# Kernel optimization log

Hardware: AMD Instinct MI355X
Metric: run time of the kernel (lower is better)

Reference implementation:

```python
import jax, jax.numpy as jnp
import numpy as np
from jax import lax

GRID = 200      # _FIXED_GRID_LEN
SOFT_K = 50.0   # _SOFT_MASK_K
BN_EPS = 1e-5


def setup_inputs() -> dict:
    key = jax.random.key(0)
    ks = jax.random.split(key, 12)
    B, L = 8192, 2001
    f32 = jnp.float32
    inp = {
        'phase': jax.random.uniform(ks[0], (B, L), f32, -1.0, 1.0),
        'primary_flux': 0.01 * jax.random.normal(ks[1], (B, L), f32),
        'secondary_flux': 0.01 * jax.random.normal(ks[2], (B, L), f32),
        'odd_even_diff': 0.01 * jax.random.normal(ks[3], (B, L), f32),
        # TaylorGateLayerV8 params
        'A': jnp.asarray(0.01, f32),
        'Bp': jnp.asarray(1.0, f32),
        't0': jnp.asarray(0.0, f32),
        # BatchNorm1d(4), eval mode (running stats)
        'bn_gamma': jnp.ones((4,), f32),
        'bn_beta': jnp.zeros((4,), f32),
        'bn_mean': jnp.zeros((4,), f32),
        'bn_var': jnp.ones((4,), f32),
        # Conv1d(4,8,7) / Conv1d(8,16,5)
        'conv1_w': 0.1 * jax.random.normal(ks[4], (8, 4, 7), f32),
        'conv1_b': jnp.zeros((8,), f32),
        'conv2_w': 0.1 * jax.random.normal(ks[5], (16, 8, 5), f32),
        'conv2_b': jnp.zeros((16,), f32),
        # Linear(21, 1)
        'fc_w': 0.1 * jax.random.normal(ks[6], (1, 21), f32),
        'fc_b': jnp.zeros((1,), f32),
    }
    return inp


def _conv1d(x, w, b, pad):
    # x: (B, C, L), w: (O, C, K)
    y = lax.conv_general_dilated(x, w, window_strides=(1,), padding=[(pad, pad)],
                                 dimension_numbers=('NCH', 'OIH', 'NCH'))
    return y + b[None, :, None]


def _interp_linear_ac(x, out_len):
    # torch F.interpolate(mode='linear', align_corners=True) on (B, L) -> (B, out_len)
    L = x.shape[1]
    pos = jnp.linspace(0.0, L - 1.0, out_len)
    i0 = jnp.floor(pos).astype(jnp.int32)
    i1 = jnp.minimum(i0 + 1, L - 1)
    w = (pos - i0).astype(x.dtype)
    return x[:, i0] * (1.0 - w) + x[:, i1] * w


def reference(phase, primary_flux, secondary_flux, odd_even_diff,
              A, Bp, t0, bn_gamma, bn_beta, bn_mean, bn_var,
              conv1_w, conv1_b, conv2_w, conv2_b, fc_w, fc_b):
    # --- TaylorGateLayerV8: 2nd-order Taylor U-shape transit template ---
    gate = -A * jnp.clip(1.0 - Bp * (phase - t0) ** 2, 0.0, None)

    # --- CNN branch ---
    x = jnp.stack([gate, primary_flux, secondary_flux, odd_even_diff], axis=1)  # (B,4,L)
    inv = bn_gamma / jnp.sqrt(bn_var + BN_EPS)
    x = x * inv[None, :, None] + (bn_beta - bn_mean * inv)[None, :, None]
    x = jax.nn.relu(_conv1d(x, conv1_w, conv1_b, 3))
    x = jax.nn.relu(_conv1d(x, conv2_w, conv2_b, 2))
    cnn_out = jnp.mean(x, axis=2)  # AdaptiveAvgPool1d(1) -> (B,16)

    # --- shape features ---
    batch = primary_flux.shape[0]
    A_abs = jnp.abs(A) + 1e-8
    depth = jnp.clip(-primary_flux, 0.0, None)
    depth_norm = depth / A_abs
    depth_rs = _interp_linear_ac(depth, GRID)  # (B, 200)
    dx = 2.0 / (GRID - 1)                       # trapz over linspace(-1,1,200)
    auc_raw = dx * (jnp.sum(depth_rs, axis=1) - 0.5 * (depth_rs[:, 0] + depth_rs[:, -1]))
    auc_norm = auc_raw / A_abs
    dip_all = jax.nn.sigmoid(SOFT_K * (depth_norm - 0.1))
    flat_bot = jax.nn.sigmoid(SOFT_K * (depth_norm - 0.8))
    ingress = dip_all - flat_bot
    total = 1.0 - dip_all + ingress + flat_bot + 1e-8
    ingress = ingress / total
    flat_bot = flat_bot / total
    t14 = jnp.mean(ingress + flat_bot, axis=1) + 1e-8
    t12_t14 = jnp.mean(ingress, axis=1) / t14
    flat_bottom = jnp.mean(flat_bot, axis=1)
    B_bcast = jnp.broadcast_to(Bp, (batch,)).astype(depth.dtype)
    shape = jnp.stack([B_bcast, auc_raw, auc_norm, t12_t14, flat_bottom], axis=1)  # (B,5)

    features = jnp.concatenate([cnn_out, shape], axis=1)  # (B,21)
    logits = features @ fc_w.T + fc_b
    return jax.nn.sigmoid(logits)
```

## Files before the change

kernel.cpp:

```cpp
#include <hip/hip_runtime.h>
#include <math.h>

#define L_LEN 2001
#define CCH 224
#define NCH 9
#define XRECS 256
#define YRECS 240
#define NTC 14

typedef __attribute__((ext_vector_type(8))) short bf16x8;
typedef __attribute__((ext_vector_type(4))) float f32x4;
typedef __attribute__((ext_vector_type(16))) float f32x16;
typedef __attribute__((ext_vector_type(4), aligned(4))) float f32x4u;
#if __has_builtin(__builtin_amdgcn_cvt_pk_bf16_f32)
typedef __attribute__((ext_vector_type(2))) __bf16 bf16x2_t;
#endif

union FragU { unsigned u[4]; uint2 u2[2]; uint4 u4; bf16x8 v; };

__device__ __forceinline__ unsigned short f2bf(float f) {
    unsigned u = __builtin_bit_cast(unsigned, f);
    u += 0x7fffu + ((u >> 16) & 1u);
    return (unsigned short)(u >> 16);
}
__device__ __forceinline__ unsigned bfpack(float lo, float hi) {
#if __has_builtin(__builtin_amdgcn_cvt_pk_bf16_f32)
    bf16x2_t r = __builtin_amdgcn_cvt_pk_bf16_f32(lo, hi);
    return __builtin_bit_cast(unsigned, r);
#else
    unsigned ul = __builtin_bit_cast(unsigned, lo);
    unsigned uh = __builtin_bit_cast(unsigned, hi);
    ul += 0x7fffu + ((ul >> 16) & 1u);
    uh += 0x7fffu + ((uh >> 16) & 1u);
    return __builtin_amdgcn_perm(uh, ul, 0x07060302);
#endif
}
__device__ __forceinline__ float fast_rcp(float x) { return __builtin_amdgcn_rcpf(x); }
__device__ __forceinline__ float fexp2(float x) {
#if __has_builtin(__builtin_amdgcn_exp2f)
    return __builtin_amdgcn_exp2f(x);
#else
    return __expf(x * 0.69314718f);
#endif
}

__global__ __launch_bounds__(256, 4)
void taylor_cnn_v10_wave(const float* __restrict__ phase, const float* __restrict__ primary,
                         const float* __restrict__ secondary, const float* __restrict__ oddeven,
                         const float* __restrict__ pA, const float* __restrict__ pBp,
                         const float* __restrict__ pT0,
                         const float* __restrict__ bng, const float* __restrict__ bnb,
                         const float* __restrict__ bnm, const float* __restrict__ bnv,
                         const float* __restrict__ w1, const float* __restrict__ b1,
                         const float* __restrict__ w2, const float* __restrict__ b2,
                         const float* __restrict__ fcw, const float* __restrict__ fcb,
                         float* __restrict__ out, int nrows)
{
    __shared__ __align__(16) unsigned int xs_i[4][XRECS * 2];
    __shared__ __align__(16) unsigned int y1_i[4][YRECS * 4];

    const int tid = threadIdx.x;
    const int l   = tid & 63;
    const int wid = tid >> 6;
    const int row = blockIdx.x * 4 + wid;
    if (row >= nrows) return;
    const long base = (long)row * L_LEN;

    unsigned int* xs = xs_i[wid];
    unsigned int* y1 = y1_i[wid];

    const int n    = l & 15;
    const int quad = l >> 4;
    const int c    = l & 31;
    const int h    = l >> 5;

    const float A  = pA[0];
    const float Bp = pBp[0];
    const float t0 = pT0[0];
    const float A_abs = fabsf(A) + 1e-8f;
    const float rAabs = 1.0f / A_abs;
    const float nBp  = -Bp;
    const float cExp = -72.134766f * rAabs;

    float inv1, inv2, inv3, gInv0, off0, off1, off2, off3;
    {
        float iv0 = bng[0] / sqrtf(bnv[0] + 1e-5f);
        float iv1 = bng[1] / sqrtf(bnv[1] + 1e-5f);
        float iv2 = bng[2] / sqrtf(bnv[2] + 1e-5f);
        float iv3 = bng[3] / sqrtf(bnv[3] + 1e-5f);
        gInv0 = -A * iv0;
        inv1 = iv1; inv2 = iv2; inv3 = iv3;
        off0 = bnb[0] - bnm[0] * iv0;
        off1 = bnb[1] - bnm[1] * iv1;
        off2 = bnb[2] - bnm[2] * iv2;
        off3 = bnb[3] - bnm[3] * iv3;
    }

    bf16x8 a32_0, a32_1;
#pragma unroll
    for (int jp = 0; jp < 8; ++jp) {
        int ch_  = jp & 3;
        int tap0 = (jp >> 2) + 2 * h;
        int tap1 = 4 + (jp >> 2) + 2 * h;
        float v0 = (c < 8) ? w1[(c * 4 + ch_) * 7 + tap0] : 0.0f;
        float v1 = (c < 8 && tap1 < 7) ? w1[(c * 4 + ch_) * 7 + tap1] : 0.0f;
        a32_0[jp] = (short)f2bf(v0);
        a32_1[jp] = (short)f2bf(v1);
    }
    f32x16 cb32;
#pragma unroll
    for (int r = 0; r < 16; ++r)
        cb32[r] = (r < 4) ? b1[(r & 3) + 4 * h] : 0.0f;

    bf16x8 a1;
#pragma unroll
    for (int jp = 0; jp < 8; ++jp) {
        int j = quad + 4 * (jp >> 2);
        int cc = jp & 3;
        float v = (n < 8 && j < 7) ? w1[(n * 4 + cc) * 7 + j] : 0.0f;
        a1[jp] = (short)f2bf(v);
    }
    bf16x8 a20, a21;
#pragma unroll
    for (int jp = 0; jp < 8; ++jp) {
        float v0 = w2[(n * 8 + jp) * 5 + quad];
        float v1 = (quad + 4 < 5) ? w2[(n * 8 + jp) * 5 + quad + 4] : 0.0f;
        a20[jp] = (short)f2bf(v0);
        a21[jp] = (short)f2bf(v1);
    }
    f32x4 cb1, cb2;
#pragma unroll
    for (int r = 0; r < 4; ++r) {
        cb1[r] = b1[(quad * 4 + r) & 7];
        cb2[r] = b2[quad * 4 + r];
    }
    float fw0 = fcw[quad * 4 + 0];
    float fw1 = fcw[quad * 4 + 1];
    float fw2 = fcw[quad * 4 + 2];
    float fw3 = fcw[quad * 4 + 3];

    float s_ing = 0.0f, s_fb = 0.0f;
    float m0 = 0.f, m1 = 0.f, m2 = 0.f, m3 = 0.f;

    float s_auc = 0.0f;
#pragma unroll
    for (int k = 0; k < 4; ++k) {
        int s = l + 64 * k;
        if (k < 3 || l < 8) {
            float pos = (float)s * (2000.0f / 199.0f);
            int i0 = (int)pos;
            if (i0 > 2000) i0 = 2000;
            int i1 = (i0 + 1 < L_LEN) ? i0 + 1 : 2000;
            float w  = pos - (float)i0;
            float d0 = fmaxf(-primary[base + i0], 0.f);
            float d1 = fmaxf(-primary[base + i1], 0.f);
            float v  = d0 * (1.0f - w) + d1 * w;
            float wt = (s == 0 || s == 199) ? 0.5f : 1.0f;
            s_auc += v * wt;
        }
    }

    auto aRec = [&](int m, int p, bool valid, bool core) {
        float ph = phase[base + p];
        float pf = primary[base + p];
        float sf = secondary[base + p];
        float oe = oddeven[base + p];
        float dd = ph - t0;
        float g  = fmaxf(fmaf(dd * dd, nBp, 1.0f), 0.0f);
        float x0 = fmaf(g,  gInv0, off0);
        float x1 = fmaf(pf, inv1, off1);
        float x2 = fmaf(sf, inv2, off2);
        float x3 = fmaf(oe, inv3, off3);
        unsigned d0 = bfpack(x0, x1);
        unsigned d1 = bfpack(x2, x3);
        if (!valid) { d0 = 0u; d1 = 0u; }
        *(uint2*)&xs[2 * m] = make_uint2(d0, d1);
        float depth = fmaxf(-pf, 0.0f);
        float e   = fexp2(depth * cExp);
        float dip = fast_rcp(fmaf(e, 148.413159f, 1.0f));
        float fb  = fast_rcp(fmaf(e, 2.35385267e17f, 1.0f));
        float ing = dip - fb;
        if (!core) { ing = 0.f; fb = 0.f; }
        s_ing += ing;
        s_fb  += fb;
    };

    const float coreMask = (l >= 4 && l < 60) ? 1.0f : 0.0f;

#pragma unroll 1
    for (int ch = 0; ch < NCH; ++ch) {
        const int c0 = ch * CCH;
        const int pb = c0 - 16;
        const bool isFirst = (ch == 0);
        const bool isLast  = (ch == NCH - 1);

        if (!isLast) {
            int p0 = pb + 4 * l;
            bool zl = false;
            if (isFirst && p0 < 0) { p0 = 0; zl = true; }
            const f32x4u ph4 = *(const f32x4u*)&phase[base + p0];
            const f32x4u pf4 = *(const f32x4u*)&primary[base + p0];
            const f32x4u sf4 = *(const f32x4u*)&secondary[base + p0];
            const f32x4u oe4 = *(const f32x4u*)&oddeven[base + p0];
            unsigned dw[8];
            float ingA = 0.f, fbA = 0.f;
#pragma unroll
            for (int j = 0; j < 4; ++j) {
                float dd = ph4[j] - t0;
                float g  = fmaxf(fmaf(dd * dd, nBp, 1.0f), 0.0f);
                float x0 = fmaf(g,      gInv0, off0);
                float x1 = fmaf(pf4[j], inv1,  off1);
                float x2 = fmaf(sf4[j], inv2,  off2);
                float x3 = fmaf(oe4[j], inv3,  off3);
                dw[2 * j]     = bfpack(x0, x1);
                dw[2 * j + 1] = bfpack(x2, x3);
                float depth = fmaxf(-pf4[j], 0.0f);
                float e   = fexp2(depth * cExp);
                float dip = fast_rcp(fmaf(e, 148.413159f, 1.0f));
                float fb  = fast_rcp(fmaf(e, 2.35385267e17f, 1.0f));
                ingA += dip - fb;
                fbA  += fb;
            }
            if (zl) {
#pragma unroll
                for (int j = 0; j < 8; ++j) dw[j] = 0u;
            }
            *(uint4*)&xs[8 * l]     = make_uint4(dw[0], dw[1], dw[2], dw[3]);
            *(uint4*)&xs[8 * l + 4] = make_uint4(dw[4], dw[5], dw[6], dw[7]);
            s_ing = fmaf(ingA, coreMask, s_ing);
            s_fb  = fmaf(fbA,  coreMask, s_fb);
        } else {
            bool v0  = (l >= 16);
            bool co0 = (l >= 16);
            int  p0s = pb + l;
            int  p3  = pb + l + 192;
            bool v3  = (l < 33);
            bool co3 = v3 && (l < 48);
            if (p3 > 2000) p3 = 2000;
            aRec(l,        p0s,          true, co0); (void)v0;
            aRec(l + 64,   pb + l + 64,  true, true);
            aRec(l + 128,  pb + l + 128, true, true);
            aRec(l + 192,  p3,           v3,   co3);
        }

        {
            const int cb = c + 2 * h + 5;
#pragma unroll 2
            for (int T = 0; T < 7; ++T) {
                const int R0 = 32 * T + cb;
                FragU b0, b1f;
                b0.u2[0]  = *(const uint2*)&xs[2 * R0];
                b0.u2[1]  = *(const uint2*)&xs[2 * R0 + 2];
                b1f.u2[0] = *(const uint2*)&xs[2 * R0 + 8];
                b1f.u2[1] = *(const uint2*)&xs[2 * R0 + 10];
                f32x16 d = __builtin_amdgcn_mfma_f32_32x32x16_bf16(a32_0, b0.v,  cb32, 0, 0, 0);
                d        = __builtin_amdgcn_mfma_f32_32x32x16_bf16(a32_1, b1f.v, d,    0, 0, 0);
                unsigned w0  = bfpack(fmaxf(d[0], 0.f), fmaxf(d[1], 0.f));
                unsigned w1_ = bfpack(fmaxf(d[2], 0.f), fmaxf(d[3], 0.f));
                if (isFirst && T == 0) {
                    if (c < 8) { w0 = 0u; w1_ = 0u; }
                }
                if (isLast && T == 6) {
                    if (c > 24) { w0 = 0u; w1_ = 0u; }
                }
                *(uint2*)&y1[4 * (32 * T + c) + 2 * h] = make_uint2(w0, w1_);
            }
            if (!isLast) {
                int qb = 224 + n + quad + 5;
                FragU bu;
                bu.u2[0] = *(const uint2*)&xs[2 * qb];
                bu.u2[1] = *(const uint2*)&xs[2 * (qb + 4)];
                f32x4 d = __builtin_amdgcn_mfma_f32_16x16x32_bf16(a1, bu.v, cb1, 0, 0, 0);
                if (l < 32) {
                    unsigned w0  = bfpack(fmaxf(d[0], 0.f), fmaxf(d[1], 0.f));
                    unsigned w1_ = bfpack(fmaxf(d[2], 0.f), fmaxf(d[3], 0.f));
                    *(uint2*)&y1[4 * (224 + n) + 2 * quad] = make_uint2(w0, w1_);
                }
            } else {
                if (l < 32)
                    *(uint2*)&y1[4 * (224 + n) + 2 * quad] = make_uint2(0u, 0u);
            }
        }

        const int maskT = isLast ? 13 : -1;
#pragma unroll 2
        for (int t = 0; t < NTC; ++t) {
            int q = 16 * t + n + quad + 6;
            FragU u0, u1;
            u0.u4 = *(const uint4*)&y1[4 * q];
            u1.u4 = *(const uint4*)&y1[4 * (q + 4)];
            f32x4 d = __builtin_amdgcn_mfma_f32_16x16x32_bf16(a20, u0.v, cb2, 0, 0, 0);
            d = __builtin_amdgcn_mfma_f32_16x16x32_bf16(a21, u1.v, d, 0, 0, 0);
            if (t == maskT) {
                float msk = (n == 0) ? 1.0f : 0.0f;
                m0 = fmaf(fmaxf(d[0], 0.f), msk, m0);
                m1 = fmaf(fmaxf(d[1], 0.f), msk, m1);
                m2 = fmaf(fmaxf(d[2], 0.f), msk, m2);
                m3 = fmaf(fmaxf(d[3], 0.f), msk, m3);
            } else {
                m0 += fmaxf(d[0], 0.f);
                m1 += fmaxf(d[1], 0.f);
                m2 += fmaxf(d[2], 0.f);
                m3 += fmaxf(d[3], 0.f);
            }
        }
    }

#pragma unroll
    for (int dlt = 8; dlt >= 1; dlt >>= 1) {
        m0 += __shfl_xor(m0, dlt);
        m1 += __shfl_xor(m1, dlt);
        m2 += __shfl_xor(m2, dlt);
        m3 += __shfl_xor(m3, dlt);
    }
    float part = m0 * fw0 + m1 * fw1 + m2 * fw2 + m3 * fw3;
    part = (n == 0) ? part : 0.0f;
    part += __shfl_xor(part, 16);
    part += __shfl_xor(part, 32);
#pragma unroll
    for (int dlt = 32; dlt >= 1; dlt >>= 1) {
        s_ing += __shfl_xor(s_ing, dlt);
        s_fb  += __shfl_xor(s_fb,  dlt);
        s_auc += __shfl_xor(s_auc, dlt);
    }

    if (l == 0) {
        float logit = fcb[0] + part * (1.0f / 2001.0f);
        float auc_raw  = (float)(2.0 / 199.0) * s_auc;
        float auc_norm = auc_raw / A_abs;
        float m_ing = s_ing / 2001.0f;
        float m_fb  = s_fb  / 2001.0f;
        float t14   = (s_ing + s_fb) / 2001.0f + 1e-8f;
        float t12   = m_ing / t14;

        logit += Bp       * fcw[16]
               + auc_raw  * fcw[17]
               + auc_norm * fcw[18]
               + t12      * fcw[19]
               + m_fb     * fcw[20];

        out[row] = 1.0f / (1.0f + expf(-logit));
    }
}

extern "C" void kernel_launch(void* const* d_in, const int* in_sizes, int n_in,
                              void* d_out, int out_size, void* d_ws, size_t ws_size,
                              hipStream_t stream) {
    const float* phase     = (const float*)d_in[0];
    const float* primary   = (const float*)d_in[1];
    const float* secondary = (const float*)d_in[2];
    const float* oddeven   = (const float*)d_in[3];
    const float* pA        = (const float*)d_in[4];
    const float* pBp       = (const float*)d_in[5];
    const float* pT0       = (const float*)d_in[6];
    const float* bng       = (const float*)d_in[7];
    const float* bnb       = (const float*)d_in[8];
    const float* bnm       = (const float*)d_in[9];
    const float* bnv       = (const float*)d_in[10];
    const float* w1        = (const float*)d_in[11];
    const float* b1        = (const float*)d_in[12];
    const float* w2        = (const float*)d_in[13];
    const float* b2        = (const float*)d_in[14];
    const float* fcw       = (const float*)d_in[15];
    const float* fcb       = (const float*)d_in[16];
    float* out = (float*)d_out;

    int nrows = in_sizes[0] / L_LEN;
    dim3 grid((nrows + 3) / 4), block(256);
    hipLaunchKernelGGL(taylor_cnn_v10_wave, grid, block, 0, stream,
                       phase, primary, secondary, oddeven, pA, pBp, pT0,
                       bng, bnb, bnm, bnv, w1, b1, w2, b2, fcw, fcb, out, nrows);
}
```

Before: 291.2 us.

## Prefetch next chunk's inputs into registers and peel last chunk out of loop

The per-row chunk loop now issues the global loads for the following chunk before computing the current one, so memory latency overlaps with the MFMA conv work. The final partial chunk is peeled into its own block, which removes the isLast branches and masks from the main loop. The ingress sum is replaced by a dip sum, with ingress recovered once at the end as dip minus flat-bottom. Register pressure rises from holding two sets of 16 floats, which could hurt occupancy under launch_bounds(256,4).

```diff
diff --git a/kernel.cpp b/kernel.cpp
--- a/kernel.cpp
+++ b/kernel.cpp
@@ -45,7 +45,7 @@
 }
 
 __global__ __launch_bounds__(256, 4)
-void taylor_cnn_v10_wave(const float* __restrict__ phase, const float* __restrict__ primary,
+void taylor_cnn_v11_wave(const float* __restrict__ phase, const float* __restrict__ primary,
                          const float* __restrict__ secondary, const float* __restrict__ oddeven,
                          const float* __restrict__ pA, const float* __restrict__ pBp,
                          const float* __restrict__ pT0,
@@ -139,7 +139,7 @@
     float fw2 = fcw[quad * 4 + 2];
     float fw3 = fcw[quad * 4 + 3];
 
-    float s_ing = 0.0f, s_fb = 0.0f;
+    float s_dip = 0.0f, s_fb = 0.0f;
     float m0 = 0.f, m1 = 0.f, m2 = 0.f, m3 = 0.f;
 
     float s_auc = 0.0f;
@@ -179,31 +179,41 @@
         float e   = fexp2(depth * cExp);
         float dip = fast_rcp(fmaf(e, 148.413159f, 1.0f));
         float fb  = fast_rcp(fmaf(e, 2.35385267e17f, 1.0f));
-        float ing = dip - fb;
-        if (!core) { ing = 0.f; fb = 0.f; }
-        s_ing += ing;
+        if (!core) { dip = 0.f; fb = 0.f; }
+        s_dip += dip;
         s_fb  += fb;
     };
 
     const float coreMask = (l >= 4 && l < 60) ? 1.0f : 0.0f;
 
+    f32x4u ph4, pf4, sf4, oe4;
+    {
+        int p0 = 4 * l - 16; if (p0 < 0) p0 = 0;
+        ph4 = *(const f32x4u*)&phase[base + p0];
+        pf4 = *(const f32x4u*)&primary[base + p0];
+        sf4 = *(const f32x4u*)&secondary[base + p0];
+        oe4 = *(const f32x4u*)&oddeven[base + p0];
+    }
+
 #pragma unroll 1
-    for (int ch = 0; ch < NCH; ++ch) {
+    for (int ch = 0; ch < NCH - 1; ++ch) {
         const int c0 = ch * CCH;
-        const int pb = c0 - 16;
         const bool isFirst = (ch == 0);
-        const bool isLast  = (ch == NCH - 1);
-
-        if (!isLast) {
-            int p0 = pb + 4 * l;
-            bool zl = false;
-            if (isFirst && p0 < 0) { p0 = 0; zl = true; }
-            const f32x4u ph4 = *(const f32x4u*)&phase[base + p0];
-            const f32x4u pf4 = *(const f32x4u*)&primary[base + p0];
-            const f32x4u sf4 = *(const f32x4u*)&secondary[base + p0];
-            const f32x4u oe4 = *(const f32x4u*)&oddeven[base + p0];
+
+        f32x4u nph, npf, nsf, noe;
+        if (ch < NCH - 2) {
+            const long pn = base + (c0 + CCH - 16 + 4 * l);
+            nph = *(const f32x4u*)&phase[pn];
+            npf = *(const f32x4u*)&primary[pn];
+            nsf = *(const f32x4u*)&secondary[pn];
+            noe = *(const f32x4u*)&oddeven[pn];
+        } else {
+            nph = ph4; npf = pf4; nsf = sf4; noe = oe4;
+        }
+
+        {
             unsigned dw[8];
-            float ingA = 0.f, fbA = 0.f;
+            float dipA = 0.f, fbA = 0.f;
 #pragma unroll
             for (int j = 0; j < 4; ++j) {
                 float dd = ph4[j] - t0;
@@ -218,29 +228,17 @@
                 float e   = fexp2(depth * cExp);
                 float dip = fast_rcp(fmaf(e, 148.413159f, 1.0f));
                 float fb  = fast_rcp(fmaf(e, 2.35385267e17f, 1.0f));
-                ingA += dip - fb;
+                dipA += dip;
                 fbA  += fb;
             }
-            if (zl) {
+            if (isFirst && l < 4) {
 #pragma unroll
                 for (int j = 0; j < 8; ++j) dw[j] = 0u;
             }
             *(uint4*)&xs[8 * l]     = make_uint4(dw[0], dw[1], dw[2], dw[3]);
             *(uint4*)&xs[8 * l + 4] = make_uint4(dw[4], dw[5], dw[6], dw[7]);
-            s_ing = fmaf(ingA, coreMask, s_ing);
+            s_dip = fmaf(dipA, coreMask, s_dip);
             s_fb  = fmaf(fbA,  coreMask, s_fb);
-        } else {
-            bool v0  = (l >= 16);
-            bool co0 = (l >= 16);
-            int  p0s = pb + l;
-            int  p3  = pb + l + 192;
-            bool v3  = (l < 33);
-            bool co3 = v3 && (l < 48);
-            if (p3 > 2000) p3 = 2000;
-            aRec(l,        p0s,          true, co0); (void)v0;
-            aRec(l + 64,   pb + l + 64,  true, true);
-            aRec(l + 128,  pb + l + 128, true, true);
-            aRec(l + 192,  p3,           v3,   co3);
         }
 
         {
@@ -260,29 +258,20 @@
                 if (isFirst && T == 0) {
                     if (c < 8) { w0 = 0u; w1_ = 0u; }
                 }
-                if (isLast && T == 6) {
-                    if (c > 24) { w0 = 0u; w1_ = 0u; }
-                }
                 *(uint2*)&y1[4 * (32 * T + c) + 2 * h] = make_uint2(w0, w1_);
             }
-            if (!isLast) {
-                int qb = 224 + n + quad + 5;
-                FragU bu;
-                bu.u2[0] = *(const uint2*)&xs[2 * qb];
-                bu.u2[1] = *(const uint2*)&xs[2 * (qb + 4)];
-                f32x4 d = __builtin_amdgcn_mfma_f32_16x16x32_bf16(a1, bu.v, cb1, 0, 0, 0);
-                if (l < 32) {
-                    unsigned w0  = bfpack(fmaxf(d[0], 0.f), fmaxf(d[1], 0.f));
-                    unsigned w1_ = bfpack(fmaxf(d[2], 0.f), fmaxf(d[3], 0.f));
-                    *(uint2*)&y1[4 * (224 + n) + 2 * quad] = make_uint2(w0, w1_);
-                }
-            } else {
-                if (l < 32)
-                    *(uint2*)&y1[4 * (224 + n) + 2 * quad] = make_uint2(0u, 0u);
-            }
-        }
-
-        const int maskT = isLast ? 13 : -1;
+            int qb = 224 + n + quad + 5;
+            FragU bu;
+            bu.u2[0] = *(const uint2*)&xs[2 * qb];
+            bu.u2[1] = *(const uint2*)&xs[2 * (qb + 4)];
+            f32x4 d = __builtin_amdgcn_mfma_f32_16x16x32_bf16(a1, bu.v, cb1, 0, 0, 0);
+            if (l < 32) {
+                unsigned w0  = bfpack(fmaxf(d[0], 0.f), fmaxf(d[1], 0.f));
+                unsigned w1_ = bfpack(fmaxf(d[2], 0.f), fmaxf(d[3], 0.f));
+                *(uint2*)&y1[4 * (224 + n) + 2 * quad] = make_uint2(w0, w1_);
+            }
+        }
+
 #pragma unroll 2
         for (int t = 0; t < NTC; ++t) {
             int q = 16 * t + n + quad + 6;
@@ -291,7 +280,61 @@
             u1.u4 = *(const uint4*)&y1[4 * (q + 4)];
             f32x4 d = __builtin_amdgcn_mfma_f32_16x16x32_bf16(a20, u0.v, cb2, 0, 0, 0);
             d = __builtin_amdgcn_mfma_f32_16x16x32_bf16(a21, u1.v, d, 0, 0, 0);
-            if (t == maskT) {
+            m0 += fmaxf(d[0], 0.f);
+            m1 += fmaxf(d[1], 0.f);
+            m2 += fmaxf(d[2], 0.f);
+            m3 += fmaxf(d[3], 0.f);
+        }
+
+        ph4 = nph; pf4 = npf; sf4 = nsf; oe4 = noe;
+    }
+
+    {
+        const int c0 = (NCH - 1) * CCH;
+        const int pb = c0 - 16;
+
+        {
+            bool co0 = (l >= 16);
+            int  p3  = pb + l + 192;
+            bool v3  = (l < 33);
+            bool co3 = v3 && (l < 48);
+            if (p3 > 2000) p3 = 2000;
+            aRec(l,        pb + l,       true, co0);
+            aRec(l + 64,   pb + l + 64,  true, true);
+            aRec(l + 128,  pb + l + 128, true, true);
+            aRec(l + 192,  p3,           v3,   co3);
+        }
+
+        {
+            const int cb = c + 2 * h + 5;
+#pragma unroll 2
+            for (int T = 0; T < 7; ++T) {
+                const int R0 = 32 * T + cb;
+                FragU b0, b1f;
+                b0.u2[0]  = *(const uint2*)&xs[2 * R0];
+                b0.u2[1]  = *(const uint2*)&xs[2 * R0 + 2];
+                b1f.u2[0] = *(const uint2*)&xs[2 * R0 + 8];
+                b1f.u2[1] = *(const uint2*)&xs[2 * R0 + 10];
+                f32x16 d = __builtin_amdgcn_mfma_f32_32x32x16_bf16(a32_0, b0.v,  cb32, 0, 0, 0);
+                d        = __builtin_amdgcn_mfma_f32_32x32x16_bf16(a32_1, b1f.v, d,    0, 0, 0);
+                unsigned w0  = bfpack(fmaxf(d[0], 0.f), fmaxf(d[1], 0.f));
+                unsigned w1_ = bfpack(fmaxf(d[2], 0.f), fmaxf(d[3], 0.f));
+                if (T == 6 && c > 24) { w0 = 0u; w1_ = 0u; }
+                *(uint2*)&y1[4 * (32 * T + c) + 2 * h] = make_uint2(w0, w1_);
+            }
+            if (l < 32)
+                *(uint2*)&y1[4 * (224 + n) + 2 * quad] = make_uint2(0u, 0u);
+        }
+
+#pragma unroll 2
+        for (int t = 0; t < NTC; ++t) {
+            int q = 16 * t + n + quad + 6;
+            FragU u0, u1;
+            u0.u4 = *(const uint4*)&y1[4 * q];
+            u1.u4 = *(const uint4*)&y1[4 * (q + 4)];
+            f32x4 d = __builtin_amdgcn_mfma_f32_16x16x32_bf16(a20, u0.v, cb2, 0, 0, 0);
+            d = __builtin_amdgcn_mfma_f32_16x16x32_bf16(a21, u1.v, d, 0, 0, 0);
+            if (t == 13) {
                 float msk = (n == 0) ? 1.0f : 0.0f;
                 m0 = fmaf(fmaxf(d[0], 0.f), msk, m0);
                 m1 = fmaf(fmaxf(d[1], 0.f), msk, m1);
@@ -319,18 +362,19 @@
     part += __shfl_xor(part, 32);
 #pragma unroll
     for (int dlt = 32; dlt >= 1; dlt >>= 1) {
-        s_ing += __shfl_xor(s_ing, dlt);
+        s_dip += __shfl_xor(s_dip, dlt);
         s_fb  += __shfl_xor(s_fb,  dlt);
         s_auc += __shfl_xor(s_auc, dlt);
     }
 
     if (l == 0) {
+        float Sing = s_dip - s_fb;
         float logit = fcb[0] + part * (1.0f / 2001.0f);
         float auc_raw  = (float)(2.0 / 199.0) * s_auc;
         float auc_norm = auc_raw / A_abs;
-        float m_ing = s_ing / 2001.0f;
+        float m_ing = Sing / 2001.0f;
         float m_fb  = s_fb  / 2001.0f;
-        float t14   = (s_ing + s_fb) / 2001.0f + 1e-8f;
+        float t14   = s_dip / 2001.0f + 1e-8f;
         float t12   = m_ing / t14;
 
         logit += Bp       * fcw[16]
@@ -367,7 +411,7 @@
 
     int nrows = in_sizes[0] / L_LEN;
     dim3 grid((nrows + 3) / 4), block(256);
-    hipLaunchKernelGGL(taylor_cnn_v10_wave, grid, block, 0, stream,
+    hipLaunchKernelGGL(taylor_cnn_v11_wave, grid, block, 0, stream,
                        phase, primary, secondary, oddeven, pA, pBp, pT0,
                        bng, bnb, bnm, bnv, w1, b1, w2, b2, fcw, fcb, out, nrows);
 }
```

Result: faster. 281.9 us (-3.2%).
